# Performance work log

Measured on AMD Instinct MI355X. Metric: run time of the kernel, lower is better.

## Reference

```python
import jax, jax.numpy as jnp
import numpy as np

DN = ('NCHW', 'OIHW', 'NCHW')
PAD1 = [(1, 1), (1, 1)]


def conv3x3(x, w):
    return jax.lax.conv_general_dilated(x, w, window_strides=(1, 1), padding=PAD1, dimension_numbers=DN)


def setup_inputs() -> dict:
    key = jax.random.key(0)
    ks = jax.random.split(key, 5)
    B, C, H, W = 8, 256, 56, 56
    return {
        'x': jax.random.normal(ks[0], (B, C, H, W), jnp.float32),
        'weight': jax.random.normal(ks[1], (C, C, 3, 3), jnp.float32) * 0.05,
        'A_w': jax.random.normal(ks[2], (1, C, 3, 3), jnp.float32),
        'se_w1': jax.random.normal(ks[3], (16, C, 3, 3), jnp.float32) * 0.02,
        'se_w2': jax.random.normal(ks[4], (1, 16, 3, 3), jnp.float32) * 0.1,
    }


def reference(x, weight, A_w, se_w1, se_w2):
    # weight = weight * A_w (A_w broadcasts over the output-channel dim)
    w = weight * A_w  # [C, C, 3, 3]
    # SE-style spatial attention map A: [B, 1, H, W]
    a = jax.nn.sigmoid(conv3x3(jax.nn.relu(conv3x3(x, se_w1)), se_w2))
    # Torch: unfold(x) * A, then matmul with flattened weight. Since A
    # broadcasts across the C*9 patch dim, this equals conv2d(x, w) * A.
    out = conv3x3(x, w) * a  # [B, C, H, W]
    return out
```

## Files before the change

### kernel.cpp

```cpp
#include <hip/hip_runtime.h>


typedef unsigned short u16;
typedef __bf16 bf16x8 __attribute__((ext_vector_type(8)));
typedef unsigned short us8 __attribute__((ext_vector_type(8)));
typedef unsigned short us4v __attribute__((ext_vector_type(4)));
typedef float f32x4 __attribute__((ext_vector_type(4)));
typedef float f4v __attribute__((ext_vector_type(4)));

#define HP 58
#define HW 3136

__device__ __forceinline__ u16 f2bf(float f) {
  unsigned u = __float_as_uint(f);
  u = (u + 0x7fffu + ((u >> 16) & 1u)) >> 16;
  return (u16)u;
}
__device__ __forceinline__ float bf2f(u16 v) {
  return __uint_as_float(((unsigned)v) << 16);
}

__device__ __forceinline__ void gload16(const u16* g, u16* l) {
  __builtin_amdgcn_global_load_lds((const __attribute__((address_space(1))) void*)g,
                                   (__attribute__((address_space(3))) void*)l,
                                   16, 0, 0);
}

__global__ __launch_bounds__(256) void k_pre(const float* __restrict__ x,
                                             const float* __restrict__ weight,
                                             const float* __restrict__ A_w,
                                             const float* __restrict__ se_w1,
                                             u16* __restrict__ xp, u16* __restrict__ wb,
                                             u16* __restrict__ w1b, u16* __restrict__ se1p) {
  __shared__ __align__(16) u16 trans[56 * 72];
  const int bid = blockIdx.x;
  const int t = threadIdx.x;
  if (bid < 448) {
    const int h = bid % 56, b = bid / 56;
    if (t < 64) {
      int half = t >> 5, seg = t & 31;
      us8 z8 = {};
      *(us8*)(xp + ((size_t)((b * HP + h + 1) * HP + half * 57)) * 256 + seg * 8) = z8;
    }
    for (int cc = 0; cc < 4; ++cc) {
      const int c0 = cc * 64;
#pragma unroll
      for (int i = 0; i < 4; ++i) {
        int idx = t + 256 * i;
        if (idx < 896) {
          int ci = idx / 14, s = idx % 14;
          f4v v = *(const f4v*)(x + ((size_t)(b * 256 + c0 + ci)) * HW + h * 56 + s * 4);
#pragma unroll
          for (int j = 0; j < 4; ++j) trans[(s * 4 + j) * 72 + ci] = f2bf(v[j]);
        }
      }
      __syncthreads();
#pragma unroll
      for (int i = 0; i < 2; ++i) {
        int idx = t + 256 * i;
        if (idx < 448) {
          int w = idx >> 3, seg = idx & 7;
          us8 v = *(const us8*)&trans[w * 72 + seg * 8];
          *(us8*)(xp + ((size_t)((b * HP + h + 1) * HP + (w + 1))) * 256 + c0 + seg * 8) = v;
        }
      }
      __syncthreads();
    }
  } else if (bid < 2896) {
    int idx = (bid - 448) * 256 + t;
    if (idx < 589824) {
      int tap = idx >> 16; int rem = idx & 65535; int o = rem >> 8; int c = rem & 255;
      wb[idx] = f2bf(weight[(o * 256 + c) * 9 + tap] * A_w[c * 9 + tap]);
    } else if (idx < 589824 + 36864) {
      int j = idx - 589824;
      int tap = j >> 12; int rem = j & 4095; int o = rem >> 8; int c = rem & 255;
      w1b[j] = f2bf(se_w1[(o * 256 + c) * 9 + tap]);
    }
  } else {
    int zid = (bid - 2896) * 256 + t;
    us8 z8 = {};
#pragma unroll
    for (int j = 0; j < 2; ++j) {
      int ch = zid + j * 45056;
      if (ch < 29696) {
        int b = ch / 3712; int rem = ch - b * 3712;
        int row = (rem < 1856) ? 0 : 57;
        int r2 = (rem < 1856) ? rem : rem - 1856;
        int col = r2 >> 5, seg = r2 & 31;
        *(us8*)(xp + ((size_t)((b * HP + row) * HP + col)) * 256 + seg * 8) = z8;
      } else if (ch < 29696 + 53824) {
        int c2 = ch - 29696;
        *(us8*)(se1p + (size_t)c2 * 8) = z8;
      }
    }
  }
}

__global__ __launch_bounds__(256) void k_se1(const u16* __restrict__ xp,
                                             const u16* __restrict__ w1b,
                                             u16* __restrict__ se1p) {
  __shared__ __align__(16) u16 Alds[144 * 8 * 8];
  __shared__ __align__(16) u16 slab[2080 * 8];
  const int t = threadIdx.x;
  const int lane = t & 63;
  const int wv = t >> 6;
  const int l15 = lane & 15, lg = lane >> 4;
  const int wg = blockIdx.x;
  const int b = wg & 7;
  const int h0 = (wg >> 3) * 2;

  f32x4 acc[2];
  f32x4 z = {0.f, 0.f, 0.f, 0.f};
  acc[0] = z; acc[1] = z;

  for (int cc = 0; cc < 4; ++cc) {
    const int c0 = cc * 64;
    __syncthreads();
    for (int idx = t; idx < 1152; idx += 256) {
      int row = idx >> 3, seg = idx & 7;
      us8 v = *(const us8*)(w1b + ((size_t)row * 256 + c0 + seg * 8));
      *(us8*)&Alds[(row * 8 + (seg ^ (row & 7))) * 8] = v;
    }
#pragma unroll
    for (int i = 0; i < 8; ++i) {
      int s_lin = wv * 512 + i * 64 + lane;
      int r = s_lin >> 9, col = (s_lin >> 3) & 63, seg = s_lin & 7;
      const u16* src = xp + ((size_t)((b * HP + h0 + r) * HP + col)) * 256 + c0 +
                       ((seg ^ (col & 7)) * 8);
      gload16(src, &slab[(wv * 512 + i * 64) * 8]);
    }
    __syncthreads();
    for (int dh = 0; dh < 3; ++dh) {
      for (int dw = 0; dw < 3; ++dw) {
        const int tap = dh * 3 + dw;
#pragma unroll
        for (int kk = 0; kk < 2; ++kk) {
          int arow = tap * 16 + l15;
          bf16x8 af = *(const bf16x8*)&Alds[(arow * 8 + ((kk * 4 + lg) ^ (arow & 7))) * 8];
#pragma unroll
          for (int nt = 0; nt < 2; ++nt) {
            int p = wv * 32 + nt * 16 + l15;
            int rr = (p >> 6) + dh, col = (p & 63) + dw;
            bf16x8 bfr = *(const bf16x8*)&slab[((rr * 64 + col) * 8 + ((kk * 4 + lg) ^ (col & 7))) * 8];
            acc[nt] = __builtin_amdgcn_mfma_f32_16x16x32_bf16(af, bfr, acc[nt], 0, 0, 0);
          }
        }
      }
    }
  }
#pragma unroll
  for (int nt = 0; nt < 2; ++nt) {
    int p = wv * 32 + nt * 16 + l15;
    int r = p >> 6, w = p & 63;
    if (w < 56) {
      us4v pk;
#pragma unroll
      for (int reg = 0; reg < 4; ++reg) {
        float v = acc[nt][reg];
        v = v > 0.f ? v : 0.f;
        pk[reg] = f2bf(v);
      }
      *(us4v*)(se1p + ((size_t)((b * HP + h0 + r + 1) * HP + (w + 1))) * 16 + lg * 4) = pk;
    }
  }
}

__global__ __launch_bounds__(256) void k_main(const u16* __restrict__ xp,
                                              const u16* __restrict__ wb,
                                              const u16* __restrict__ se1p,
                                              const float* __restrict__ se_w2,
                                              float* __restrict__ out) {
  __shared__ __align__(16) u16 slab[4 * 64 * 8 * 8];
  __shared__ __align__(16) u16 Albuf[2][128 * 64];
  __shared__ float w2s[144];
  __shared__ float amap_s[128];
  const int t = threadIdx.x;
  const int lane = t & 63;
  const int wid = t >> 6;
  const int wm = wid >> 1;
  const int wn = wid & 1;
  const int l15 = lane & 15, lg = lane >> 4;
  const int lrow = lane >> 3, lseg = lane & 7;
  const int wg = blockIdx.x;
  const int b = wg & 7;
  const int rem = wg >> 3;
  const int h0 = (rem >> 1) * 2;
  const int mbase = (rem & 1) * 128;

  if (t < 144) w2s[t] = se_w2[t];

  f32x4 acc[4][4];
  f32x4 z = {0.f, 0.f, 0.f, 0.f};
#pragma unroll
  for (int mt = 0; mt < 4; ++mt)
#pragma unroll
    for (int nt = 0; nt < 4; ++nt) acc[mt][nt] = z;

  auto stage_slab = [&](int cc) {
    const int c0 = cc * 64;
#pragma unroll
    for (int i = 0; i < 8; ++i) {
      int chunk = wid * 512 + i * 64 + lane;
      int row = chunk >> 9, col = (chunk >> 3) & 63, seg = chunk & 7;
      const u16* src = xp + ((size_t)((b * HP + h0 + row) * HP + col)) * 256 + c0 +
                       ((seg ^ (col & 7)) * 8);
      gload16(src, &slab[(wid * 512 + i * 64) * 8]);
    }
  };
  auto stage_A = [&](int tap, int cc, int buf) {
    const int c0 = cc * 64;
#pragma unroll
    for (int i = 0; i < 4; ++i) {
      int li = wid * 4 + i;
      int row = li * 8 + lrow;
      const u16* src = wb + ((size_t)(tap * 256 + mbase + row)) * 256 + c0 +
                       ((lseg ^ (row & 7)) * 8);
      gload16(src, &Albuf[buf][li * 512]);
    }
  };

  stage_slab(0);
  stage_A(0, 0, 0);
  int pb = 0;
  for (int cc = 0; cc < 4; ++cc) {
    for (int tap = 0; tap < 9; ++tap) {
      if (tap < 8) {
        stage_A(tap + 1, cc, pb ^ 1);
        asm volatile("s_waitcnt vmcnt(4)" ::: "memory");
      } else {
        asm volatile("s_waitcnt vmcnt(0)" ::: "memory");
      }
      __builtin_amdgcn_s_barrier();
      __builtin_amdgcn_sched_barrier(0);
      const int dh = tap / 3, dw = tap % 3;
#pragma unroll
      for (int kk = 0; kk < 2; ++kk) {
        bf16x8 af[4], bfr[4];
#pragma unroll
        for (int mt = 0; mt < 4; ++mt) {
          int row = wm * 64 + mt * 16 + l15;
          af[mt] = *(const bf16x8*)&Albuf[pb][row * 64 + (((kk * 4 + lg) ^ (row & 7)) * 8)];
        }
#pragma unroll
        for (int nt = 0; nt < 4; ++nt) {
          int p = wn * 64 + nt * 16 + l15;
          int r = (p >> 6) + dh;
          int col = ((p & 63) + dw) & 63;
          bfr[nt] = *(const bf16x8*)&slab[((r * 64 + col) * 8 + ((kk * 4 + lg) ^ (col & 7))) * 8];
        }
#pragma unroll
        for (int mt = 0; mt < 4; ++mt)
#pragma unroll
          for (int nt = 0; nt < 4; ++nt)
            acc[mt][nt] = __builtin_amdgcn_mfma_f32_16x16x32_bf16(af[mt], bfr[nt], acc[mt][nt], 0, 0, 0);
      }
      __builtin_amdgcn_sched_barrier(0);
      __builtin_amdgcn_s_barrier();
      if (tap < 8) {
        pb ^= 1;
      } else if (cc < 3) {
        stage_slab(cc + 1);
        stage_A(0, cc + 1, pb);
      }
    }
  }
  if (t < 112) {
    int r = t / 56, w = t - r * 56;
    int h = h0 + r;
    float s = 0.f;
    for (int dh2 = 0; dh2 < 3; ++dh2) {
#pragma unroll
      for (int dw2 = 0; dw2 < 3; ++dw2) {
        const u16* src = se1p + ((size_t)((b * HP + h + dh2) * HP + (w + dw2))) * 16;
        us8 v0 = *(const us8*)src;
        us8 v1 = *(const us8*)(src + 8);
        int tap = dh2 * 3 + dw2;
#pragma unroll
        for (int ci = 0; ci < 8; ++ci) s += bf2f(v0[ci]) * w2s[ci * 9 + tap];
#pragma unroll
        for (int ci = 0; ci < 8; ++ci) s += bf2f(v1[ci]) * w2s[(8 + ci) * 9 + tap];
      }
    }
    amap_s[t] = 1.f / (1.f + expf(-s));
  }
  __syncthreads();
#pragma unroll
  for (int nt = 0; nt < 4; ++nt) {
    int n = wn * 64 + nt * 16 + l15;
    int r = n >> 6, w = n & 63;
    if (w < 56) {
      float av = amap_s[r * 56 + w];
#pragma unroll
      for (int mt = 0; mt < 4; ++mt) {
        int obase = mbase + wm * 64 + mt * 16 + lg * 4;
#pragma unroll
        for (int reg = 0; reg < 4; ++reg) {
          out[((size_t)(b * 256 + obase + reg) * 56 + h0 + r) * 56 + w] = acc[mt][nt][reg] * av;
        }
      }
    }
  }
}

extern "C" void kernel_launch(void* const* d_in, const int* in_sizes, int n_in,
                              void* d_out, int out_size, void* d_ws, size_t ws_size,
                              hipStream_t stream) {
  const float* x      = (const float*)d_in[0];
  const float* weight = (const float*)d_in[1];
  const float* A_w    = (const float*)d_in[2];
  const float* se_w1  = (const float*)d_in[3];
  const float* se_w2  = (const float*)d_in[4];
  float* out = (float*)d_out;

  char* ws = (char*)d_ws;
  u16* xp   = (u16*)ws;
  u16* se1p = (u16*)(ws + 13778944);
  u16* wb   = (u16*)(ws + 14640128);
  u16* w1b  = (u16*)(ws + 15819776);

  k_pre<<<dim3(3072), dim3(256), 0, stream>>>(x, weight, A_w, se_w1, xp, wb, w1b, se1p);
  k_se1<<<dim3(224), dim3(256), 0, stream>>>(xp, w1b, se1p);
  k_main<<<dim3(448), dim3(256), 0, stream>>>(xp, wb, se1p, se_w2, out);
}
```

Before: 171.4 us.

## Register-stage weight tiles in main conv and split SE conv per row

In k_main, the double-buffered LDS weight tile loaded with global_load_lds is replaced by a single LDS buffer. The next tap's weights are prefetched into registers and written to LDS after a barrier, and the se_w2/amap scratch now aliases the slab. This cuts LDS per block to raise occupancy, at the cost of extra __syncthreads per tap and more register pressure. k_se1 now handles one output row per block over 448 blocks instead of two rows over 224, which spreads the work across more of the GPU.

```diff
diff --git a/kernel.cpp b/kernel.cpp
--- a/kernel.cpp
+++ b/kernel.cpp
@@ -99,19 +99,17 @@
 __global__ __launch_bounds__(256) void k_se1(const u16* __restrict__ xp,
                                              const u16* __restrict__ w1b,
                                              u16* __restrict__ se1p) {
-  __shared__ __align__(16) u16 Alds[144 * 8 * 8];
-  __shared__ __align__(16) u16 slab[2080 * 8];
+  __shared__ __align__(16) u16 Alds[144 * 64];
+  __shared__ __align__(16) u16 slab[3 * 64 * 64];
   const int t = threadIdx.x;
   const int lane = t & 63;
   const int wv = t >> 6;
   const int l15 = lane & 15, lg = lane >> 4;
   const int wg = blockIdx.x;
   const int b = wg & 7;
-  const int h0 = (wg >> 3) * 2;
-
-  f32x4 acc[2];
-  f32x4 z = {0.f, 0.f, 0.f, 0.f};
-  acc[0] = z; acc[1] = z;
+  const int h = wg >> 3;
+
+  f32x4 acc = {0.f, 0.f, 0.f, 0.f};
 
   for (int cc = 0; cc < 4; ++cc) {
     const int c0 = cc * 64;
@@ -119,49 +117,40 @@
     for (int idx = t; idx < 1152; idx += 256) {
       int row = idx >> 3, seg = idx & 7;
       us8 v = *(const us8*)(w1b + ((size_t)row * 256 + c0 + seg * 8));
-      *(us8*)&Alds[(row * 8 + (seg ^ (row & 7))) * 8] = v;
-    }
-#pragma unroll
-    for (int i = 0; i < 8; ++i) {
-      int s_lin = wv * 512 + i * 64 + lane;
-      int r = s_lin >> 9, col = (s_lin >> 3) & 63, seg = s_lin & 7;
-      const u16* src = xp + ((size_t)((b * HP + h0 + r) * HP + col)) * 256 + c0 +
+      *(us8*)&Alds[row * 64 + (seg ^ (row & 7)) * 8] = v;
+    }
+#pragma unroll
+    for (int i = 0; i < 6; ++i) {
+      int chunk = i * 256 + t;
+      int row = chunk >> 9, col = (chunk >> 3) & 63, seg = chunk & 7;
+      const u16* src = xp + ((size_t)((b * HP + h + row) * HP + col)) * 256 + c0 +
                        ((seg ^ (col & 7)) * 8);
-      gload16(src, &slab[(wv * 512 + i * 64) * 8]);
+      gload16(src, &slab[(i * 256 + wv * 64) * 8]);
     }
     __syncthreads();
-    for (int dh = 0; dh < 3; ++dh) {
-      for (int dw = 0; dw < 3; ++dw) {
-        const int tap = dh * 3 + dw;
-#pragma unroll
-        for (int kk = 0; kk < 2; ++kk) {
-          int arow = tap * 16 + l15;
-          bf16x8 af = *(const bf16x8*)&Alds[(arow * 8 + ((kk * 4 + lg) ^ (arow & 7))) * 8];
-#pragma unroll
-          for (int nt = 0; nt < 2; ++nt) {
-            int p = wv * 32 + nt * 16 + l15;
-            int rr = (p >> 6) + dh, col = (p & 63) + dw;
-            bf16x8 bfr = *(const bf16x8*)&slab[((rr * 64 + col) * 8 + ((kk * 4 + lg) ^ (col & 7))) * 8];
-            acc[nt] = __builtin_amdgcn_mfma_f32_16x16x32_bf16(af, bfr, acc[nt], 0, 0, 0);
-          }
-        }
-      }
-    }
-  }
-#pragma unroll
-  for (int nt = 0; nt < 2; ++nt) {
-    int p = wv * 32 + nt * 16 + l15;
-    int r = p >> 6, w = p & 63;
-    if (w < 56) {
-      us4v pk;
-#pragma unroll
-      for (int reg = 0; reg < 4; ++reg) {
-        float v = acc[nt][reg];
-        v = v > 0.f ? v : 0.f;
-        pk[reg] = f2bf(v);
-      }
-      *(us4v*)(se1p + ((size_t)((b * HP + h0 + r + 1) * HP + (w + 1))) * 16 + lg * 4) = pk;
-    }
+#pragma unroll
+    for (int tap = 0; tap < 9; ++tap) {
+      const int dh = tap / 3, dw = tap % 3;
+#pragma unroll
+      for (int kk = 0; kk < 2; ++kk) {
+        int arow = tap * 16 + l15;
+        bf16x8 af = *(const bf16x8*)&Alds[arow * 64 + (((kk * 4 + lg) ^ (arow & 7))) * 8];
+        int col = ((wv * 16 + l15) + dw) & 63;
+        bf16x8 bfr = *(const bf16x8*)&slab[((dh * 64 + col) * 8 + ((kk * 4 + lg) ^ (col & 7))) * 8];
+        acc = __builtin_amdgcn_mfma_f32_16x16x32_bf16(af, bfr, acc, 0, 0, 0);
+      }
+    }
+  }
+  int w = wv * 16 + l15;
+  if (w < 56) {
+    us4v pk;
+#pragma unroll
+    for (int reg = 0; reg < 4; ++reg) {
+      float v = acc[reg];
+      v = v > 0.f ? v : 0.f;
+      pk[reg] = f2bf(v);
+    }
+    *(us4v*)(se1p + ((size_t)((b * HP + h + 1) * HP + (w + 1))) * 16 + lg * 4) = pk;
   }
 }
 
@@ -170,10 +159,11 @@
                                               const u16* __restrict__ se1p,
                                               const float* __restrict__ se_w2,
                                               float* __restrict__ out) {
-  __shared__ __align__(16) u16 slab[4 * 64 * 8 * 8];
-  __shared__ __align__(16) u16 Albuf[2][128 * 64];
-  __shared__ float w2s[144];
-  __shared__ float amap_s[128];
+  __shared__ __align__(16) u16 S[24576];
+  u16* slab  = S;
+  u16* Albuf = S + 16384;
+  float* w2s    = (float*)S;
+  float* amap_s = (float*)(S + 512);
   const int t = threadIdx.x;
   const int lane = t & 63;
   const int wid = t >> 6;
@@ -187,14 +177,14 @@
   const int h0 = (rem >> 1) * 2;
   const int mbase = (rem & 1) * 128;
 
-  if (t < 144) w2s[t] = se_w2[t];
-
   f32x4 acc[4][4];
-  f32x4 z = {0.f, 0.f, 0.f, 0.f};
 #pragma unroll
   for (int mt = 0; mt < 4; ++mt)
 #pragma unroll
-    for (int nt = 0; nt < 4; ++nt) acc[mt][nt] = z;
+    for (int nt = 0; nt < 4; ++nt) {
+      f32x4 z = {0.f, 0.f, 0.f, 0.f};
+      acc[mt][nt] = z;
+    }
 
   auto stage_slab = [&](int cc) {
     const int c0 = cc * 64;
@@ -207,31 +197,36 @@
       gload16(src, &slab[(wid * 512 + i * 64) * 8]);
     }
   };
-  auto stage_A = [&](int tap, int cc, int buf) {
+  auto loadA = [&](int tap, int cc, us8* ra) {
     const int c0 = cc * 64;
 #pragma unroll
     for (int i = 0; i < 4; ++i) {
-      int li = wid * 4 + i;
-      int row = li * 8 + lrow;
-      const u16* src = wb + ((size_t)(tap * 256 + mbase + row)) * 256 + c0 +
-                       ((lseg ^ (row & 7)) * 8);
-      gload16(src, &Albuf[buf][li * 512]);
+      int row = wid * 32 + i * 8 + lrow;
+      ra[i] = *(const us8*)(wb + ((size_t)(tap * 256 + mbase + row)) * 256 + c0 + lseg * 8);
     }
   };
-
-  stage_slab(0);
-  stage_A(0, 0, 0);
-  int pb = 0;
+  auto writeA = [&](const us8* ra) {
+#pragma unroll
+    for (int i = 0; i < 4; ++i) {
+      int row = wid * 32 + i * 8 + lrow;
+      *(us8*)&Albuf[row * 64 + (lseg ^ (row & 7)) * 8] = ra[i];
+    }
+  };
+
+  {
+    us8 ra[4];
+    loadA(0, 0, ra);
+    stage_slab(0);
+    writeA(ra);
+    __syncthreads();
+  }
+
   for (int cc = 0; cc < 4; ++cc) {
+#pragma unroll
     for (int tap = 0; tap < 9; ++tap) {
-      if (tap < 8) {
-        stage_A(tap + 1, cc, pb ^ 1);
-        asm volatile("s_waitcnt vmcnt(4)" ::: "memory");
-      } else {
-        asm volatile("s_waitcnt vmcnt(0)" ::: "memory");
-      }
-      __builtin_amdgcn_s_barrier();
-      __builtin_amdgcn_sched_barrier(0);
+      const bool haveNext = !(cc == 3 && tap == 8);
+      us8 ra[4];
+      if (haveNext) loadA(tap < 8 ? tap + 1 : 0, tap < 8 ? cc : cc + 1, ra);
       const int dh = tap / 3, dw = tap % 3;
 #pragma unroll
       for (int kk = 0; kk < 2; ++kk) {
@@ -239,7 +234,7 @@
 #pragma unroll
         for (int mt = 0; mt < 4; ++mt) {
           int row = wm * 64 + mt * 16 + l15;
-          af[mt] = *(const bf16x8*)&Albuf[pb][row * 64 + (((kk * 4 + lg) ^ (row & 7)) * 8)];
+          af[mt] = *(const bf16x8*)&Albuf[row * 64 + (((kk * 4 + lg) ^ (row & 7))) * 8];
         }
 #pragma unroll
         for (int nt = 0; nt < 4; ++nt) {
@@ -254,16 +249,17 @@
           for (int nt = 0; nt < 4; ++nt)
             acc[mt][nt] = __builtin_amdgcn_mfma_f32_16x16x32_bf16(af[mt], bfr[nt], acc[mt][nt], 0, 0, 0);
       }
-      __builtin_amdgcn_sched_barrier(0);
-      __builtin_amdgcn_s_barrier();
-      if (tap < 8) {
-        pb ^= 1;
-      } else if (cc < 3) {
-        stage_slab(cc + 1);
-        stage_A(0, cc + 1, pb);
-      }
-    }
-  }
+      __syncthreads();
+      if (haveNext) {
+        writeA(ra);
+        if (tap == 8) stage_slab(cc + 1);
+        __syncthreads();
+      }
+    }
+  }
+
+  if (t < 144) w2s[t] = se_w2[t];
+  __syncthreads();
   if (t < 112) {
     int r = t / 56, w = t - r * 56;
     int h = h0 + r;
@@ -319,6 +315,6 @@
   u16* w1b  = (u16*)(ws + 15819776);
 
   k_pre<<<dim3(3072), dim3(256), 0, stream>>>(x, weight, A_w, se_w1, xp, wb, w1b, se1p);
-  k_se1<<<dim3(224), dim3(256), 0, stream>>>(xp, w1b, se1p);
+  k_se1<<<dim3(448), dim3(256), 0, stream>>>(xp, w1b, se1p);
   k_main<<<dim3(448), dim3(256), 0, stream>>>(xp, wb, se1p, se_w2, out);
 }
```

Result: faster. 160.3 us (-6.5%).
